# Kernel optimization log

Measured on AMD Instinct MI355X. Metric: run time of the kernel, lower is better.

The kernel has to match this reference:

```python
import jax, jax.numpy as jnp
import numpy as np

N = 50000      # nodes
E = 800000     # edges
F_IN = 128     # in_channels
HID = 128      # hidden = out channels
H = 4          # heads
C = HID // H   # per-head dim = 32
L = 3          # transformer layers (num_gat_layers=2 -> 3 convs)
G = 50         # graphs in batch
ED = 2         # edge_dim
EPS_BN = 1e-5


def setup_inputs() -> dict:
    key = jax.random.key(0)
    ks = jax.random.split(key, 24)
    s = 0.05
    f32 = jnp.float32
    inp = {
        "x": jax.random.normal(ks[0], (N, F_IN), f32),
        "edge_index": jax.random.randint(ks[1], (2, E), 0, N, dtype=jnp.int32).astype(jnp.int64),
        "edge_attr": jax.random.uniform(ks[2], (E, ED), f32),
        "batch": jnp.sort(jax.random.randint(ks[3], (N,), 0, G, dtype=jnp.int32).astype(jnp.int64)),
        # stacked per-layer TransformerConv params (all layers 128->128)
        "Wq": jax.random.normal(ks[4], (L, HID, HID), f32) * s,
        "bq": jnp.zeros((L, HID), f32),
        "Wk": jax.random.normal(ks[5], (L, HID, HID), f32) * s,
        "bk": jnp.zeros((L, HID), f32),
        "Wv": jax.random.normal(ks[6], (L, HID, HID), f32) * s,
        "bv": jnp.zeros((L, HID), f32),
        "We": jax.random.normal(ks[7], (L, ED, HID), f32) * s,
        "be": jnp.zeros((L, HID), f32),
        "Wskip": jax.random.normal(ks[8], (L, HID, HID), f32) * s,
        "bskip": jnp.zeros((L, HID), f32),
        "Wbeta": jax.random.normal(ks[9], (L, 3 * HID, 1), f32) * s,  # lin_beta: bias=False
        "bn_gamma": jnp.ones((L, HID), f32),
        "bn_beta": jnp.zeros((L, HID), f32),
        "Wout": jax.random.normal(ks[10], (HID, 1), f32) * s,
        "bout": jnp.zeros((1,), f32),
        "out_bias": jnp.zeros((1,), f32),
    }
    return inp


def reference(x, edge_index, edge_attr, batch, Wq, bq, Wk, bk, Wv, bv, We, be,
              Wskip, bskip, Wbeta, bn_gamma, bn_beta, Wout, bout, out_bias):
    src, dst = edge_index[0], edge_index[1]  # message j->i: src=j, dst=i
    scale = 1.0 / np.sqrt(C)
    for l in range(L):
        q = (x @ Wq[l] + bq[l]).reshape(N, H, C)
        k = (x @ Wk[l] + bk[l]).reshape(N, H, C)
        v = (x @ Wv[l] + bv[l]).reshape(N, H, C)
        e = (edge_attr @ We[l] + be[l]).reshape(E, H, C)
        kj = k[src] + e                                        # [E,H,C] key + edge emb
        alpha = jnp.einsum('ehc,ehc->eh', q[dst], kj) * scale  # [E,H]
        # segment softmax over incoming edges of each destination node
        amax = jax.ops.segment_max(alpha, dst, num_segments=N)
        ex = jnp.exp(alpha - amax[dst])
        den = jax.ops.segment_sum(ex, dst, num_segments=N)
        w = ex / (den[dst] + 1e-16)                            # [E,H] (dropout: eval mode)
        msg = (v[src] + e) * w[:, :, None]                     # [E,H,C]
        out = jax.ops.segment_sum(msg, dst, num_segments=N).reshape(N, HID)
        # beta-gated skip connection
        x_r = x @ Wskip[l] + bskip[l]
        gate = jax.nn.sigmoid(jnp.concatenate([out, x_r, out - x_r], axis=-1) @ Wbeta[l])
        out = gate * x_r + (1.0 - gate) * out
        # BatchNorm1d over nodes (training statistics, biased variance)
        mu = out.mean(axis=0)
        var = out.var(axis=0)
        out = (out - mu) / jnp.sqrt(var + EPS_BN) * bn_gamma[l] + bn_beta[l]
        x = jax.nn.elu(out)
    # global mean pool readout per graph
    cnt = jax.ops.segment_sum(jnp.ones((N,), x.dtype), batch, num_segments=G)
    h_G = jax.ops.segment_sum(x, batch, num_segments=G) / jnp.maximum(cnt, 1.0)[:, None]
    return h_G @ Wout + bout + out_bias  # [G,1]
```

## Files before the change

kernel.cpp:

```cpp
#include <hip/hip_runtime.h>
#include <hip/hip_fp16.h>
#include <math.h>

#define NN 50000
#define EE 800000
#define HIDDEN 128
#define NGRAPH 50
#define GEMM_TILES ((NN + 63) / 64)
#define NB_ATTN 12500

typedef _Float16 half8 __attribute__((ext_vector_type(8)));
typedef float f32x4 __attribute__((ext_vector_type(4)));

__global__ void k_degprep(const int* __restrict__ eidx, int* __restrict__ cnt,
                          int* __restrict__ rank,
                          const float* __restrict__ Wq, const float* __restrict__ Wk,
                          const float* __restrict__ Wv, const float* __restrict__ Ws,
                          _Float16* __restrict__ wt) {
    int b = blockIdx.x;
    int t = threadIdx.x;
    if (b < 3125) {
        int e = b * 256 + t;
        if (e < EE) {
            int p = atomicAdd(&cnt[eidx[EE + e]], 1);
            rank[e] = p;
        }
    } else {
        int idx = (b - 3125) * 256 + t;
        if (idx < 12 * 16384) {
            int mat = idx >> 14;
            int l = mat >> 2, w = mat & 3;
            int nk = idx & 16383;
            int n = nk >> 7, k = nk & 127;
            const float* W = (w == 0 ? Wq : w == 1 ? Wk : w == 2 ? Wv : Ws) + (size_t)l * 16384;
            wt[idx] = (_Float16)W[k * 128 + n];
        }
    }
}

__global__ void k_scan(int* __restrict__ cnt, int* __restrict__ row_ptr,
                       float* __restrict__ bn_acc3, float* __restrict__ gsum,
                       int* __restrict__ gcnt) {
    __shared__ int wsum[16];
    __shared__ int carry_s;
    int t = threadIdx.x;
    int lane = t & 63, w = t >> 6;
    if (t < 768) bn_acc3[t] = 0.f;
    if (t < 64) { gsum[t] = 0.f; gcnt[t] = 0; }
    if (t == 0) carry_s = 0;
    __syncthreads();
    for (int base = 0; base < NN; base += 4096) {
        int i0 = base + t * 4;
        int v[4];
#pragma unroll
        for (int j = 0; j < 4; j++) v[j] = (i0 + j < NN) ? cnt[i0 + j] : 0;
        int s4 = v[0] + v[1] + v[2] + v[3];
        int s = s4;
#pragma unroll
        for (int o = 1; o < 64; o <<= 1) {
            int u = __shfl_up(s, o);
            if (lane >= o) s += u;
        }
        if (lane == 63) wsum[w] = s;
        __syncthreads();
        if (w == 0) {
            int ws = (lane < 16) ? wsum[lane] : 0;
#pragma unroll
            for (int o = 1; o < 16; o <<= 1) {
                int u = __shfl_up(ws, o);
                if (lane >= o) ws += u;
            }
            if (lane < 16) wsum[lane] = ws;
        }
        __syncthreads();
        int wpre = (w == 0) ? 0 : wsum[w - 1];
        int run = carry_s + wpre + s - s4;
#pragma unroll
        for (int j = 0; j < 4; j++) {
            if (i0 + j < NN) { row_ptr[i0 + j] = run; cnt[i0 + j] = 0; run += v[j]; }
        }
        __syncthreads();
        if (t == 0) carry_s += wsum[15];
        __syncthreads();
    }
    if (t == 0) row_ptr[NN] = carry_s;
}

__device__ __forceinline__ void gemm_tile(
    const float* __restrict__ X, const _Float16* __restrict__ wt,
    const float* __restrict__ bq, const float* __restrict__ bk,
    const float* __restrict__ bv, const float* __restrict__ bs,
    const float* ab_s, int use_ab, _Float16 (*xs)[136],
    float* __restrict__ qo, unsigned int* __restrict__ kvb, float* __restrict__ xro,
    int m0)
{
    int t = threadIdx.x;
    int lane = t & 63, wid = t >> 6;
#pragma unroll
    for (int i = 0; i < 8; ++i) {
        int f = t + 256 * i;
        int r = f >> 5, c4 = (f & 31) << 2;
        float4 val = make_float4(0.f, 0.f, 0.f, 0.f);
        if (m0 + r < NN) val = *(const float4*)&X[(size_t)(m0 + r) * 128 + c4];
        if (use_ab) {
            float4 a = *(const float4*)&ab_s[c4];
            float4 bb = *(const float4*)&ab_s[128 + c4];
            float z;
            z = fmaf(val.x, a.x, bb.x); val.x = z > 0.f ? z : expm1f(z);
            z = fmaf(val.y, a.y, bb.y); val.y = z > 0.f ? z : expm1f(z);
            z = fmaf(val.z, a.z, bb.z); val.z = z > 0.f ? z : expm1f(z);
            z = fmaf(val.w, a.w, bb.w); val.w = z > 0.f ? z : expm1f(z);
        }
        _Float16* dst = &xs[r][c4];
        dst[0] = (_Float16)val.x; dst[1] = (_Float16)val.y;
        dst[2] = (_Float16)val.z; dst[3] = (_Float16)val.w;
    }
    __syncthreads();
    int quad = lane >> 4, l15 = lane & 15;
    int mrow = wid * 16;
    half8 afrag[4];
#pragma unroll
    for (int kk = 0; kk < 4; kk++)
        afrag[kk] = *(const half8*)&xs[mrow + l15][kk * 32 + quad * 8];

#pragma unroll
    for (int nt = 0; nt < 8; nt++) {
        int c = nt * 16 + l15;
        f32x4 acc[4];
#pragma unroll
        for (int w = 0; w < 4; w++) acc[w] = (f32x4){0.f, 0.f, 0.f, 0.f};
#pragma unroll
        for (int kk = 0; kk < 4; kk++) {
            half8 bf[4];
#pragma unroll
            for (int w = 0; w < 4; w++)
                bf[w] = *(const half8*)&wt[(size_t)w * 16384 + c * 128 + kk * 32 + quad * 8];
#pragma unroll
            for (int w = 0; w < 4; w++)
                acc[w] = __builtin_amdgcn_mfma_f32_16x16x32_f16(afrag[kk], bf[w], acc[w], 0, 0, 0);
        }
        float bqv = bq[c], bkv = bk[c], bvv = bv[c], bsv = bs[c];
        int nodebase = m0 + mrow + quad * 4;
#pragma unroll
        for (int r = 0; r < 4; r++) {
            int node = nodebase + r;
            bool ok = node < NN;
            float qv = acc[0][r] + bqv;
            float xv = acc[3][r] + bsv;
            float kf = acc[1][r] + bkv;
            float vf = acc[2][r] + bvv;
            float kf1 = __shfl_xor(kf, 1);
            float vf1 = __shfl_xor(vf, 1);
            if (ok) {
                qo[(size_t)node * 128 + c] = qv;
                xro[(size_t)node * 128 + c] = xv;
                if (!(lane & 1)) {
                    int w2 = __builtin_amdgcn_cvt_pk_fp8_f32(kf, kf1, 0, false);
                    w2 = __builtin_amdgcn_cvt_pk_fp8_f32(vf, vf1, w2, true);
                    kvb[(size_t)node * 64 + (c >> 1)] = (unsigned int)w2;
                }
            }
        }
    }
}

__global__ __launch_bounds__(256) void k_gemm0scat(
    const float* __restrict__ X, const _Float16* __restrict__ wt,
    const float* __restrict__ bq, const float* __restrict__ bk,
    const float* __restrict__ bv, const float* __restrict__ bs,
    float* __restrict__ qo, unsigned int* __restrict__ kvb, float* __restrict__ xro,
    const int* __restrict__ eidx, const float* __restrict__ eattr,
    const int* __restrict__ row_ptr, const int* __restrict__ rank,
    float4* __restrict__ erec)
{
    __shared__ _Float16 xs[64][136];
    int b = blockIdx.x;
    if (b < GEMM_TILES) {
        gemm_tile(X, wt, bq, bk, bv, bs, nullptr, 0, xs, qo, kvb, xro, b * 64);
    } else {
        int e = (b - GEMM_TILES) * 256 + threadIdx.x;
        if (e < EE) {
            int d = eidx[EE + e];
            int s = eidx[e];
            int rk = rank[e];
            float2 ea = *(const float2*)&eattr[2 * (size_t)e];
            int pos = row_ptr[d] + rk;
            erec[pos] = make_float4(ea.x, ea.y, __int_as_float(s), 0.f);
        }
    }
}

__global__ __launch_bounds__(256) void k_gemm4(
    const float* __restrict__ X, const _Float16* __restrict__ wt,
    const float* __restrict__ bq, const float* __restrict__ bk,
    const float* __restrict__ bv, const float* __restrict__ bs,
    const float* __restrict__ bn_acc, const float* __restrict__ gamma,
    const float* __restrict__ beta,
    float* __restrict__ qo, unsigned int* __restrict__ kvb, float* __restrict__ xro)
{
    __shared__ _Float16 xs[64][136];
    __shared__ float ab_s[256];
    int t = threadIdx.x;
    if (t < 128) {
        float mu = bn_acc[t] * (1.f / NN);
        float var = bn_acc[128 + t] * (1.f / NN) - mu * mu;
        float inv = rsqrtf(var + 1e-5f);
        float a = inv * gamma[t];
        ab_s[t] = a;
        ab_s[128 + t] = beta[t] - mu * a;
    }
    __syncthreads();
    gemm_tile(X, wt, bq, bk, bv, bs, ab_s, 1, xs, qo, kvb, xro, blockIdx.x * 64);
}

__device__ __forceinline__ float row_sum16(float p) {
    p += __int_as_float(__builtin_amdgcn_update_dpp(0, __float_as_int(p), 0x128, 0xF, 0xF, true));
    p += __int_as_float(__builtin_amdgcn_update_dpp(0, __float_as_int(p), 0x124, 0xF, 0xF, true));
    p += __int_as_float(__builtin_amdgcn_update_dpp(0, __float_as_int(p), 0x122, 0xF, 0xF, true));
    p += __int_as_float(__builtin_amdgcn_update_dpp(0, __float_as_int(p), 0x121, 0xF, 0xF, true));
    return p;
}

__global__ __launch_bounds__(256) void k_attn(
    const float* __restrict__ q, const unsigned int* __restrict__ kvb,
    const float* __restrict__ xr,
    const float4* __restrict__ erec,
    const int* __restrict__ row_ptr,
    const float* __restrict__ We, const float* __restrict__ be,
    const float* __restrict__ Wb,
    float* __restrict__ out2, float* __restrict__ bnp)
{
    __shared__ float4 es[4][64];
    int t = threadIdx.x;
    int lane = t & 63;
    int wid = t >> 6;
    int n = blockIdx.x * 4 + wid;
    int ch = lane * 2;
    float2 we0 = *(const float2*)&We[ch];
    float2 we1 = *(const float2*)&We[128 + ch];
    float2 beL = *(const float2*)&be[ch];
    const float scale = 0.17677669529663687f;

    int rs = __builtin_amdgcn_readfirstlane(row_ptr[n]);
    int re = __builtin_amdgcn_readfirstlane(row_ptr[n + 1]);
    float2 qv = *(const float2*)&q[(size_t)n * 128 + ch];
    float2 xv = *(const float2*)&xr[(size_t)n * 128 + ch];
    float den = 0.f, ax = 0.f, ay = 0.f;

    for (int cb = rs; cb < re; cb += 64) {
        int cnum = re - cb; if (cnum > 64) cnum = 64;
        int mi = cb + lane;
        if (mi < re) es[wid][lane] = erec[mi];
        int cm1 = cnum - 1;
        int ng = (cnum + 7) >> 3;
        unsigned int kkA[8], kkB[8];

#define LOAD8(KK, B0) do {                                                   \
        _Pragma("unroll")                                                    \
        for (int j = 0; j < 8; j++) {                                        \
            int o = (B0) + j; int oc = o < cm1 ? o : cm1;                    \
            int s = __float_as_int(es[wid][oc].z);                           \
            KK[j] = kvb[(size_t)(unsigned)s * 64 + lane];                    \
        }                                                                    \
    } while (0)

#define COMP8(KK, B0) do {                                                   \
        _Pragma("unroll")                                                    \
        for (int j = 0; j < 8; j++) {                                        \
            int o = (B0) + j; int oc = o < cm1 ? o : cm1;                    \
            float4 rec = es[wid][oc];                                        \
            auto kf = __builtin_amdgcn_cvt_pk_f32_fp8((int)KK[j], false);    \
            auto vf = __builtin_amdgcn_cvt_pk_f32_fp8((int)KK[j], true);     \
            float ex_ = fmaf(rec.x, we0.x, fmaf(rec.y, we1.x, beL.x));       \
            float ey_ = fmaf(rec.x, we0.y, fmaf(rec.y, we1.y, beL.y));       \
            float p = qv.x * (kf[0] + ex_) + qv.y * (kf[1] + ey_);           \
            p = row_sum16(p);                                                \
            float exv = (o < cnum) ? __expf(p * scale) : 0.f;                \
            den += exv;                                                      \
            ax = fmaf(exv, vf[0] + ex_, ax);                                 \
            ay = fmaf(exv, vf[1] + ey_, ay);                                 \
        }                                                                    \
    } while (0)

        LOAD8(kkA, 0);
        __builtin_amdgcn_sched_barrier(0);
        int g = 0;
        for (;;) {
            if (g + 1 < ng) { LOAD8(kkB, (g + 1) * 8); __builtin_amdgcn_sched_barrier(0); }
            COMP8(kkA, g * 8);
            ++g; if (g >= ng) break;
            if (g + 1 < ng) { LOAD8(kkA, (g + 1) * 8); __builtin_amdgcn_sched_barrier(0); }
            COMP8(kkB, g * 8);
            ++g; if (g >= ng) break;
        }
#undef LOAD8
#undef COMP8
    }

    float rden = 1.f / (den + 1e-16f);
    ax *= rden; ay *= rden;
    float2 wb_o = *(const float2*)&Wb[ch];
    float2 wb_r = *(const float2*)&Wb[128 + ch];
    float2 wb_d = *(const float2*)&Wb[256 + ch];
    float gp = ax * wb_o.x + ay * wb_o.y + xv.x * wb_r.x + xv.y * wb_r.y
             + (ax - xv.x) * wb_d.x + (ay - xv.y) * wb_d.y;
    gp = row_sum16(gp);
    gp += __shfl_xor(gp, 16);
    gp += __shfl_xor(gp, 32);
    float gate = 1.f / (1.f + __expf(-gp));
    float ox = gate * xv.x + (1.f - gate) * ax;
    float oy = gate * xv.y + (1.f - gate) * ay;
    *(float2*)&out2[(size_t)n * 128 + ch] = make_float2(ox, oy);

    __shared__ float s_sum[2][256], s_sq[2][256];
    s_sum[0][t] = ox; s_sum[1][t] = oy;
    s_sq[0][t] = ox * ox;  s_sq[1][t] = oy * oy;
    __syncthreads();
    if (t < 64) {
        float sx = s_sum[0][t] + s_sum[0][64 + t] + s_sum[0][128 + t] + s_sum[0][192 + t];
        float sy = s_sum[1][t] + s_sum[1][64 + t] + s_sum[1][128 + t] + s_sum[1][192 + t];
        float qx = s_sq[0][t] + s_sq[0][64 + t] + s_sq[0][128 + t] + s_sq[0][192 + t];
        float qy = s_sq[1][t] + s_sq[1][64 + t] + s_sq[1][128 + t] + s_sq[1][192 + t];
        float2* bp = (float2*)&bnp[(size_t)blockIdx.x * 256];
        bp[t] = make_float2(sx, sy);
        bp[64 + t] = make_float2(qx, qy);
    }
}

__global__ __launch_bounds__(256) void k_bnred(const float* __restrict__ part,
                                               float* __restrict__ bn_acc) {
    int t = threadIdx.x;
    int g = blockIdx.x;
    float s = 0.f;
    for (int r = g * 50; r < g * 50 + 50; ++r)
        s += part[(size_t)r * 256 + t];
    atomicAdd(&bn_acc[t], s);
}

__global__ __launch_bounds__(256) void k_pool(const float* __restrict__ x,
                                              const float* __restrict__ bn_acc,
                                              const float* __restrict__ gamma,
                                              const float* __restrict__ beta,
                                              const float* __restrict__ Wout,
                                              const int* __restrict__ batch,
                                              float* __restrict__ gsum, int* __restrict__ gcnt) {
    __shared__ float lsum[NGRAPH];
    __shared__ int lcnt[NGRAPH];
    __shared__ float ab_s[256];
    int t = threadIdx.x;
    if (t < NGRAPH) { lsum[t] = 0.f; lcnt[t] = 0; }
    if (t < 128) {
        float mu = bn_acc[t] * (1.f / NN);
        float var = bn_acc[128 + t] * (1.f / NN) - mu * mu;
        float inv = rsqrtf(var + 1e-5f);
        float a = inv * gamma[t];
        ab_s[t] = a;
        ab_s[128 + t] = beta[t] - mu * a;
    }
    __syncthreads();
    int lane = t & 63;
    int wid = t >> 6;
    int ch = lane * 2;
    float2 wo = *(const float2*)&Wout[ch];
    float2 a = *(const float2*)&ab_s[ch];
    float2 b = *(const float2*)&ab_s[128 + ch];
    for (int chunk = 0; chunk < 10; ++chunk) {
        int base = blockIdx.x * 160 + chunk * 16 + wid * 4;
        float2 xv[4];
#pragma unroll
        for (int i = 0; i < 4; i++) {
            int n = base + i;
            xv[i] = (n < NN) ? *(const float2*)&x[(size_t)n * 128 + ch]
                             : make_float2(0.f, 0.f);
        }
#pragma unroll
        for (int i = 0; i < 4; i++) {
            int n = base + i;
            if (n < NN) {
                float z0 = fmaf(xv[i].x, a.x, b.x); z0 = z0 > 0.f ? z0 : expm1f(z0);
                float z1 = fmaf(xv[i].y, a.y, b.y); z1 = z1 > 0.f ? z1 : expm1f(z1);
                float p = z0 * wo.x + z1 * wo.y;
                p += __shfl_xor(p, 1);
                p += __shfl_xor(p, 2);
                p += __shfl_xor(p, 4);
                p += __shfl_xor(p, 8);
                p += __shfl_xor(p, 16);
                p += __shfl_xor(p, 32);
                if (lane == 0) {
                    int g = batch[n];
                    atomicAdd(&lsum[g], p);
                    atomicAdd(&lcnt[g], 1);
                }
            }
        }
    }
    __syncthreads();
    if (t < NGRAPH && lcnt[t] > 0) {
        atomicAdd(&gsum[t], lsum[t]);
        atomicAdd(&gcnt[t], lcnt[t]);
    }
}

__global__ void k_final(const float* __restrict__ gsum, const int* __restrict__ gcnt,
                        const float* __restrict__ bout, const float* __restrict__ obias,
                        float* __restrict__ out) {
    int g = threadIdx.x;
    if (g < NGRAPH) out[g] = gsum[g] / fmaxf((float)gcnt[g], 1.f) + bout[0] + obias[0];
}

extern "C" void kernel_launch(void* const* d_in, const int* in_sizes, int n_in,
                              void* d_out, int out_size, void* d_ws, size_t ws_size,
                              hipStream_t stream) {
    const float* x_in       = (const float*)d_in[0];
    const int* eidx         = (const int*)d_in[1];
    const float* eattr      = (const float*)d_in[2];
    const int* batch        = (const int*)d_in[3];
    const float* Wq         = (const float*)d_in[4];
    const float* bq         = (const float*)d_in[5];
    const float* Wk         = (const float*)d_in[6];
    const float* bk         = (const float*)d_in[7];
    const float* Wv         = (const float*)d_in[8];
    const float* bv         = (const float*)d_in[9];
    const float* We         = (const float*)d_in[10];
    const float* be         = (const float*)d_in[11];
    const float* Wskip      = (const float*)d_in[12];
    const float* bskip      = (const float*)d_in[13];
    const float* Wbeta      = (const float*)d_in[14];
    const float* bn_gamma   = (const float*)d_in[15];
    const float* bn_beta    = (const float*)d_in[16];
    const float* Wout       = (const float*)d_in[17];
    const float* bout       = (const float*)d_in[18];
    const float* obias      = (const float*)d_in[19];
    float* out = (float*)d_out;

    char* ws = (char*)d_ws;
    size_t off = 0;
    auto alloc = [&](size_t bytes) -> void* {
        off = (off + 255) & ~(size_t)255;
        void* p = ws + off;
        off += bytes;
        return p;
    };
    const size_t NF = (size_t)NN * 128 * sizeof(float);
    float* xbuf    = (float*)alloc(NF);
    float* qb      = (float*)alloc(NF);
    float* xrb     = (float*)alloc(NF);
    unsigned int* kvb = (unsigned int*)alloc((size_t)NN * 64 * sizeof(unsigned int));
    _Float16* wt   = (_Float16*)alloc((size_t)12 * 16384 * sizeof(_Float16));
    int* row_ptr   = (int*)alloc((NN + 1) * sizeof(int));
    int* cnt       = (int*)alloc(NN * sizeof(int));
    int* rank      = (int*)alloc(EE * sizeof(int));
    float4* erec   = (float4*)alloc((size_t)EE * sizeof(float4));
    float* bn_acc3 = (float*)alloc(3 * 256 * sizeof(float));
    float* bnpart  = (float*)alloc((size_t)NB_ATTN * 256 * sizeof(float));
    float* gsum    = (float*)alloc(64 * sizeof(float));
    int* gcnt      = (int*)alloc(64 * sizeof(int));
    (void)ws_size; (void)n_in; (void)in_sizes; (void)out_size;

    hipMemsetAsync(cnt, 0, NN * sizeof(int), stream);
    k_degprep<<<3125 + 768, 256, 0, stream>>>(eidx, cnt, rank, Wq, Wk, Wv, Wskip, wt);
    k_scan<<<1, 1024, 0, stream>>>(cnt, row_ptr, bn_acc3, gsum, gcnt);

    k_gemm0scat<<<GEMM_TILES + 3125, 256, 0, stream>>>(
        x_in, wt, bq, bk, bv, bskip, qb, kvb, xrb,
        eidx, eattr, row_ptr, rank, erec);
    k_attn<<<NB_ATTN, 256, 0, stream>>>(
        qb, kvb, xrb, erec, row_ptr,
        We, be, Wbeta, xbuf, bnpart);
    k_bnred<<<250, 256, 0, stream>>>(bnpart, bn_acc3);

    for (int l = 1; l < 3; ++l) {
        k_gemm4<<<GEMM_TILES, 256, 0, stream>>>(
            xbuf, wt + (size_t)l * 65536,
            bq + l * 128, bk + l * 128, bv + l * 128, bskip + l * 128,
            bn_acc3 + (l - 1) * 256, bn_gamma + (l - 1) * 128, bn_beta + (l - 1) * 128,
            qb, kvb, xrb);
        k_attn<<<NB_ATTN, 256, 0, stream>>>(
            qb, kvb, xrb, erec, row_ptr,
            We + (size_t)l * 256, be + l * 128, Wbeta + (size_t)l * 384,
            xbuf, bnpart);
        k_bnred<<<250, 256, 0, stream>>>(bnpart, bn_acc3 + l * 256);
    }

    k_pool<<<313, 256, 0, stream>>>(xbuf, bn_acc3 + 2 * 256,
                                    bn_gamma + 2 * 128, bn_beta + 2 * 128,
                                    Wout, batch, gsum, gcnt);
    k_final<<<1, 64, 0, stream>>>(gsum, gcnt, bout, obias, out);
}
```

Measured before the change: 609.9 us.

## Compact edge records, store q in fp16, and factor edge embedding out of attention loop

Edge records shrink from 16-byte float4 to 8-byte packed (src index plus fp16 edge attributes) and are written with nontemporal stores, and q is stored in fp16 instead of fp32. In the attention kernel, the edge-embedding contribution is folded algebraically: q·We is precomputed per node, and edge-attribute-weighted sums are accumulated and expanded once after the loop. The scale is folded into q with log2e so exp2 can be used directly. These changes cut memory traffic and per-edge ALU work, at the cost of reduced precision for q and the edge attributes.

```diff
diff --git a/kernel.cpp b/kernel.cpp
--- a/kernel.cpp
+++ b/kernel.cpp
@@ -10,7 +10,9 @@
 #define NB_ATTN 12500
 
 typedef _Float16 half8 __attribute__((ext_vector_type(8)));
+typedef _Float16 half2v __attribute__((ext_vector_type(2)));
 typedef float f32x4 __attribute__((ext_vector_type(4)));
+typedef unsigned long long u64;
 
 __global__ void k_degprep(const int* __restrict__ eidx, int* __restrict__ cnt,
                           int* __restrict__ rank,
@@ -91,7 +93,7 @@
     const float* __restrict__ bq, const float* __restrict__ bk,
     const float* __restrict__ bv, const float* __restrict__ bs,
     const float* ab_s, int use_ab, _Float16 (*xs)[136],
-    float* __restrict__ qo, unsigned int* __restrict__ kvb, float* __restrict__ xro,
+    _Float16* __restrict__ qo, unsigned int* __restrict__ kvb, float* __restrict__ xro,
     int m0)
 {
     int t = threadIdx.x;
@@ -152,7 +154,7 @@
             float kf1 = __shfl_xor(kf, 1);
             float vf1 = __shfl_xor(vf, 1);
             if (ok) {
-                qo[(size_t)node * 128 + c] = qv;
+                qo[(size_t)node * 128 + c] = (_Float16)qv;
                 xro[(size_t)node * 128 + c] = xv;
                 if (!(lane & 1)) {
                     int w2 = __builtin_amdgcn_cvt_pk_fp8_f32(kf, kf1, 0, false);
@@ -168,10 +170,10 @@
     const float* __restrict__ X, const _Float16* __restrict__ wt,
     const float* __restrict__ bq, const float* __restrict__ bk,
     const float* __restrict__ bv, const float* __restrict__ bs,
-    float* __restrict__ qo, unsigned int* __restrict__ kvb, float* __restrict__ xro,
+    _Float16* __restrict__ qo, unsigned int* __restrict__ kvb, float* __restrict__ xro,
     const int* __restrict__ eidx, const float* __restrict__ eattr,
     const int* __restrict__ row_ptr, const int* __restrict__ rank,
-    float4* __restrict__ erec)
+    u64* __restrict__ erec)
 {
     __shared__ _Float16 xs[64][136];
     int b = blockIdx.x;
@@ -184,8 +186,11 @@
             int s = eidx[e];
             int rk = rank[e];
             float2 ea = *(const float2*)&eattr[2 * (size_t)e];
+            union { _Float16 h[2]; unsigned int u; } cv;
+            cv.h[0] = (_Float16)ea.x; cv.h[1] = (_Float16)ea.y;
             int pos = row_ptr[d] + rk;
-            erec[pos] = make_float4(ea.x, ea.y, __int_as_float(s), 0.f);
+            u64 rec = ((u64)cv.u << 32) | (unsigned int)s;
+            __builtin_nontemporal_store(rec, &erec[pos]);
         }
     }
 }
@@ -196,7 +201,7 @@
     const float* __restrict__ bv, const float* __restrict__ bs,
     const float* __restrict__ bn_acc, const float* __restrict__ gamma,
     const float* __restrict__ beta,
-    float* __restrict__ qo, unsigned int* __restrict__ kvb, float* __restrict__ xro)
+    _Float16* __restrict__ qo, unsigned int* __restrict__ kvb, float* __restrict__ xro)
 {
     __shared__ _Float16 xs[64][136];
     __shared__ float ab_s[256];
@@ -222,15 +227,15 @@
 }
 
 __global__ __launch_bounds__(256) void k_attn(
-    const float* __restrict__ q, const unsigned int* __restrict__ kvb,
+    const _Float16* __restrict__ q, const unsigned int* __restrict__ kvb,
     const float* __restrict__ xr,
-    const float4* __restrict__ erec,
+    const u64* __restrict__ erec,
     const int* __restrict__ row_ptr,
     const float* __restrict__ We, const float* __restrict__ be,
     const float* __restrict__ Wb,
     float* __restrict__ out2, float* __restrict__ bnp)
 {
-    __shared__ float4 es[4][64];
+    __shared__ u64 es[4][64];
     int t = threadIdx.x;
     int lane = t & 63;
     int wid = t >> 6;
@@ -239,18 +244,23 @@
     float2 we0 = *(const float2*)&We[ch];
     float2 we1 = *(const float2*)&We[128 + ch];
     float2 beL = *(const float2*)&be[ch];
-    const float scale = 0.17677669529663687f;
+    const float S2 = 0.17677669529663687f * 1.4426950408889634f;
 
     int rs = __builtin_amdgcn_readfirstlane(row_ptr[n]);
     int re = __builtin_amdgcn_readfirstlane(row_ptr[n + 1]);
-    float2 qv = *(const float2*)&q[(size_t)n * 128 + ch];
+    half2v qh = *(const half2v*)&q[(size_t)n * 128 + ch];
     float2 xv = *(const float2*)&xr[(size_t)n * 128 + ch];
-    float den = 0.f, ax = 0.f, ay = 0.f;
+    float2 qs; qs.x = (float)qh[0] * S2; qs.y = (float)qh[1] * S2;
+    float qw0 = qs.x * we0.x + qs.y * we0.y;
+    float qw1 = qs.x * we1.x + qs.y * we1.y;
+    float qb0 = qs.x * beL.x + qs.y * beL.y;
+    float den = 0.f, sA = 0.f, sB = 0.f, ax = 0.f, ay = 0.f;
 
     for (int cb = rs; cb < re; cb += 64) {
         int cnum = re - cb; if (cnum > 64) cnum = 64;
         int mi = cb + lane;
         if (mi < re) es[wid][lane] = erec[mi];
+        const unsigned int* es32 = (const unsigned int*)&es[wid][0];
         int cm1 = cnum - 1;
         int ng = (cnum + 7) >> 3;
         unsigned int kkA[8], kkB[8];
@@ -259,8 +269,8 @@
         _Pragma("unroll")                                                    \
         for (int j = 0; j < 8; j++) {                                        \
             int o = (B0) + j; int oc = o < cm1 ? o : cm1;                    \
-            int s = __float_as_int(es[wid][oc].z);                           \
-            KK[j] = kvb[(size_t)(unsigned)s * 64 + lane];                    \
+            unsigned int s = es32[oc * 2];                                   \
+            KK[j] = kvb[(size_t)s * 64 + lane];                              \
         }                                                                    \
     } while (0)
 
@@ -268,17 +278,23 @@
         _Pragma("unroll")                                                    \
         for (int j = 0; j < 8; j++) {                                        \
             int o = (B0) + j; int oc = o < cm1 ? o : cm1;                    \
-            float4 rec = es[wid][oc];                                        \
+            union { unsigned int u; _Float16 h[2]; } cv;                     \
+            cv.u = es32[oc * 2 + 1];                                         \
+            float eax = (float)cv.h[0], eay = (float)cv.h[1];                \
             auto kf = __builtin_amdgcn_cvt_pk_f32_fp8((int)KK[j], false);    \
             auto vf = __builtin_amdgcn_cvt_pk_f32_fp8((int)KK[j], true);     \
-            float ex_ = fmaf(rec.x, we0.x, fmaf(rec.y, we1.x, beL.x));       \
-            float ey_ = fmaf(rec.x, we0.y, fmaf(rec.y, we1.y, beL.y));       \
-            float p = qv.x * (kf[0] + ex_) + qv.y * (kf[1] + ey_);           \
+            float p = qs.x * kf[0];                                          \
+            p = fmaf(qs.y, kf[1], p);                                        \
+            p = fmaf(eax, qw0, p);                                           \
+            p = fmaf(eay, qw1, p);                                           \
+            p += qb0;                                                        \
             p = row_sum16(p);                                                \
-            float exv = (o < cnum) ? __expf(p * scale) : 0.f;                \
+            float exv = (o < cnum) ? __builtin_amdgcn_exp2f(p) : 0.f;        \
             den += exv;                                                      \
-            ax = fmaf(exv, vf[0] + ex_, ax);                                 \
-            ay = fmaf(exv, vf[1] + ey_, ay);                                 \
+            sA = fmaf(exv, eax, sA);                                         \
+            sB = fmaf(exv, eay, sB);                                         \
+            ax = fmaf(exv, vf[0], ax);                                       \
+            ay = fmaf(exv, vf[1], ay);                                       \
         }                                                                    \
     } while (0)
 
@@ -297,19 +313,21 @@
 #undef COMP8
     }
 
+    float axT = ax + sA * we0.x + sB * we1.x + den * beL.x;
+    float ayT = ay + sA * we0.y + sB * we1.y + den * beL.y;
     float rden = 1.f / (den + 1e-16f);
-    ax *= rden; ay *= rden;
+    float axs = axT * rden, ays = ayT * rden;
     float2 wb_o = *(const float2*)&Wb[ch];
     float2 wb_r = *(const float2*)&Wb[128 + ch];
     float2 wb_d = *(const float2*)&Wb[256 + ch];
-    float gp = ax * wb_o.x + ay * wb_o.y + xv.x * wb_r.x + xv.y * wb_r.y
-             + (ax - xv.x) * wb_d.x + (ay - xv.y) * wb_d.y;
+    float gp = axs * wb_o.x + ays * wb_o.y + xv.x * wb_r.x + xv.y * wb_r.y
+             + (axs - xv.x) * wb_d.x + (ays - xv.y) * wb_d.y;
     gp = row_sum16(gp);
     gp += __shfl_xor(gp, 16);
     gp += __shfl_xor(gp, 32);
     float gate = 1.f / (1.f + __expf(-gp));
-    float ox = gate * xv.x + (1.f - gate) * ax;
-    float oy = gate * xv.y + (1.f - gate) * ay;
+    float ox = gate * xv.x + (1.f - gate) * axs;
+    float oy = gate * xv.y + (1.f - gate) * ays;
     *(float2*)&out2[(size_t)n * 128 + ch] = make_float2(ox, oy);
 
     __shared__ float s_sum[2][256], s_sq[2][256];
@@ -443,14 +461,14 @@
     };
     const size_t NF = (size_t)NN * 128 * sizeof(float);
     float* xbuf    = (float*)alloc(NF);
-    float* qb      = (float*)alloc(NF);
+    _Float16* qb   = (_Float16*)alloc((size_t)NN * 128 * sizeof(_Float16));
     float* xrb     = (float*)alloc(NF);
     unsigned int* kvb = (unsigned int*)alloc((size_t)NN * 64 * sizeof(unsigned int));
     _Float16* wt   = (_Float16*)alloc((size_t)12 * 16384 * sizeof(_Float16));
     int* row_ptr   = (int*)alloc((NN + 1) * sizeof(int));
     int* cnt       = (int*)alloc(NN * sizeof(int));
     int* rank      = (int*)alloc(EE * sizeof(int));
-    float4* erec   = (float4*)alloc((size_t)EE * sizeof(float4));
+    u64* erec      = (u64*)alloc((size_t)EE * sizeof(u64));
     float* bn_acc3 = (float*)alloc(3 * 256 * sizeof(float));
     float* bnpart  = (float*)alloc((size_t)NB_ATTN * 256 * sizeof(float));
     float* gsum    = (float*)alloc(64 * sizeof(float));
```

Result: no change. 614.5 us (+0.8%).
